# Performance work log

Hardware: AMD Instinct MI355X
Metric: run time of the kernel (lower is better)

Reference implementation:

```python
import jax, jax.numpy as jnp
import numpy as np

BS, CIN, COUT, KS, H, W = 16, 256, 256, 3, 80, 80
HID = CIN // 16   # Attention hidden = in_planes // ratio(16)
K = 5             # len(angle_list)
TEMP = 30.0       # attention temperature

# Spatial permutations replicating AdaptiveAngleConv._rotate_kernel for 3x3 kernels.
# perm[dest_flat] = source_flat (flat = 3*row + col).
_PERMS = {
    45:  np.array([3, 0, 1, 6, 4, 2, 7, 8, 5]),
    90:  np.array([6, 3, 0, 7, 4, 1, 8, 5, 2]),
    135: np.array([7, 6, 3, 8, 4, 0, 5, 2, 1]),
    180: np.array([8, 7, 6, 5, 4, 3, 2, 1, 0]),
}

def _rotate(w, angle):
    o, i = w.shape[:2]
    return w.reshape(o, i, 9)[..., _PERMS[angle]].reshape(o, i, 3, 3)

def setup_inputs() -> dict:
    key = jax.random.key(0)
    ks = jax.random.split(key, 9)
    s = lambda fan: 1.0 / np.sqrt(fan)
    return {
        "x":       jax.random.normal(ks[0], (BS, CIN, H, W), jnp.float32),
        "w_base":  jax.random.normal(ks[1], (COUT, CIN, KS, KS), jnp.float32) * s(CIN * KS * KS),
        "b_base":  jax.random.normal(ks[2], (COUT,), jnp.float32) * 0.1,
        "b_extra": jax.random.normal(ks[3], (K - 1, COUT), jnp.float32) * 0.1,
        "w_net":   jax.random.normal(ks[4], (HID, CIN), jnp.float32) * s(CIN),
        "w_nfc":   jax.random.normal(ks[5], (K, HID), jnp.float32) * s(HID),
        "w_cin":   jax.random.normal(ks[6], (CIN, HID), jnp.float32) * s(HID),
        "w_k2":    jax.random.normal(ks[7], (KS * KS, HID), jnp.float32) * s(HID),
        "w_out":   jax.random.normal(ks[8], (COUT, HID), jnp.float32) * s(HID),
    }

def reference(x, w_base, b_base, b_extra, w_net, w_nfc, w_cin, w_k2, w_out):
    bs = x.shape[0]
    # Attention: global-avg-pool then 1x1 convs == matmuls on pooled vectors
    pooled = x.mean(axis=(2, 3))                                   # [bs, Cin]
    h = jax.nn.relu(pooled @ w_net.T)                              # [bs, HID]
    n_att   = jax.nn.softmax((h @ w_nfc.T) / TEMP, axis=-1)        # [bs, K]
    cin_att = jax.nn.sigmoid(h @ w_cin.T)                          # [bs, Cin]
    k2_att  = jax.nn.sigmoid(h @ w_k2.T).reshape(bs, 1, 1, KS, KS) # [bs,1,1,ks,ks]
    out_att = jax.nn.sigmoid(h @ w_out.T)                          # [bs, Cout]

    # K rotated kernel variants: [K, Cout, Cin, ks, ks]
    k_sum = jnp.stack([w_base, _rotate(w_base, 45), _rotate(w_base, 90),
                       _rotate(w_base, 135), _rotate(w_base, 180)], axis=0)
    b_sum = jnp.concatenate([b_base[None], b_extra], axis=0)       # [K, Cout]

    # Per-sample dynamic weight synthesis
    agg_w = jnp.einsum('bk,koicd->boicd', n_att, k_sum)            # [bs,Cout,Cin,ks,ks]
    agg_w = (agg_w
             * cin_att[:, None, :, None, None]
             * k2_att
             * out_att[:, :, None, None, None])
    agg_b = n_att @ b_sum                                          # [bs, Cout]

    # Per-sample conv (== F.conv2d with groups=bs trick)
    def conv1(xi, wi, bi):
        y = jax.lax.conv_general_dilated(
            xi[None], wi, window_strides=(1, 1), padding=((1, 1), (1, 1)),
            dimension_numbers=('NCHW', 'OIHW', 'NCHW'))[0]
        return y + bi[:, None, None]

    return jax.vmap(conv1)(x, agg_w, agg_b)                        # [bs,Cout,H,W]
```

## Files before the change

### kernel.cpp

```cpp
#include <hip/hip_runtime.h>
#include <hip/hip_bf16.h>
#include <cstdint>
#include <cstddef>

#define BS   16
#define CIN  256
#define COUT 256
#define HID  16
#define KNUM 5
#define TEMP 30.0f
#define NPIX 6400

typedef _Float16 half8 __attribute__((ext_vector_type(8)));
typedef float    f32x4 __attribute__((ext_vector_type(4)));

__device__ __forceinline__ void gload_lds16(const void* g, void* l) {
    __builtin_amdgcn_global_load_lds(
        (const __attribute__((address_space(1))) unsigned int*)g,
        (__attribute__((address_space(3))) unsigned int*)l, 16, 0, 0);
}

__global__ void zero_pool_kernel(float* __restrict__ pooled) {
    pooled[blockIdx.x * 256 + threadIdx.x] = 0.f;
}

__global__ __launch_bounds__(256)
void xpose_kernel(const float* __restrict__ x, _Float16* __restrict__ xt,
                  float* __restrict__ pooled) {
    const int b = blockIdx.y, p0 = blockIdx.x * 64, c = threadIdx.x;
    const float* xp = x + ((size_t)(b * CIN + c)) * NPIX + p0;
    _Float16* tp = xt + ((size_t)b * NPIX + p0) * CIN + c;
    float s = 0.f;
    #pragma unroll
    for (int k0 = 0; k0 < 64; k0 += 16) {
        float4 v[4];
        #pragma unroll
        for (int q = 0; q < 4; ++q) v[q] = *(const float4*)(xp + k0 + q * 4);
        #pragma unroll
        for (int q = 0; q < 4; ++q) {
            s += v[q].x + v[q].y + v[q].z + v[q].w;
            tp[(size_t)(k0 + q * 4 + 0) * CIN] = (_Float16)v[q].x;
            tp[(size_t)(k0 + q * 4 + 1) * CIN] = (_Float16)v[q].y;
            tp[(size_t)(k0 + q * 4 + 2) * CIN] = (_Float16)v[q].z;
            tp[(size_t)(k0 + q * 4 + 3) * CIN] = (_Float16)v[q].w;
        }
    }
    atomicAdd(&pooled[b * CIN + c], s);
}

__global__ void attn_kernel(const float* __restrict__ pooled,
                            const float* __restrict__ b_base,
                            const float* __restrict__ b_extra,
                            const float* __restrict__ w_net,
                            const float* __restrict__ w_nfc,
                            const float* __restrict__ w_cin,
                            const float* __restrict__ w_k2,
                            const float* __restrict__ w_out,
                            float* __restrict__ cin_att,
                            float* __restrict__ out_att,
                            float* __restrict__ agg_b,
                            float* __restrict__ coef,
                            float pool_scale) {
    const int b = blockIdx.x;
    const int t = threadIdx.x;
    __shared__ float sp[CIN];
    __shared__ float sh[HID];
    __shared__ float sn[KNUM];
    __shared__ float sk2[9];

    sp[t] = pooled[b * CIN + t] * pool_scale;
    __syncthreads();

    if (t < HID) {
        float a = 0.f;
        for (int c = 0; c < CIN; ++c) a += sp[c] * w_net[t * CIN + c];
        sh[t] = fmaxf(a, 0.f);
    }
    __syncthreads();

    if (t == 0) {
        float l[KNUM], m = -1e30f;
        for (int k = 0; k < KNUM; ++k) {
            float a = 0.f;
            for (int j = 0; j < HID; ++j) a += sh[j] * w_nfc[k * HID + j];
            l[k] = a / TEMP;
            m = fmaxf(m, l[k]);
        }
        float ssum = 0.f;
        for (int k = 0; k < KNUM; ++k) { l[k] = __expf(l[k] - m); ssum += l[k]; }
        for (int k = 0; k < KNUM; ++k) sn[k] = l[k] / ssum;
    }
    if (t < 9) {
        float a = 0.f;
        for (int j = 0; j < HID; ++j) a += sh[j] * w_k2[t * HID + j];
        sk2[t] = 1.f / (1.f + __expf(-a));
    }
    __syncthreads();

    {
        float a = 0.f, o = 0.f;
        for (int j = 0; j < HID; ++j) {
            a += sh[j] * w_cin[t * HID + j];
            o += sh[j] * w_out[t * HID + j];
        }
        cin_att[b * CIN + t] = 1.f / (1.f + __expf(-a));
        out_att[b * COUT + t] = 1.f / (1.f + __expf(-o));
        float bb = sn[0] * b_base[t];
        for (int k = 1; k < KNUM; ++k) bb += sn[k] * b_extra[(k - 1) * COUT + t];
        agg_b[b * COUT + t] = bb;
    }

    if (t < 81) {
        const int P45[9]  = {3, 0, 1, 6, 4, 2, 7, 8, 5};
        const int P90[9]  = {6, 3, 0, 7, 4, 1, 8, 5, 2};
        const int P135[9] = {7, 6, 3, 8, 4, 0, 5, 2, 1};
        const int P180[9] = {8, 7, 6, 5, 4, 3, 2, 1, 0};
        const int d = t / 9, s = t % 9;
        float c = 0.f;
        if (d == s)        c += sn[0];
        if (P45[d]  == s)  c += sn[1];
        if (P90[d]  == s)  c += sn[2];
        if (P135[d] == s)  c += sn[3];
        if (P180[d] == s)  c += sn[4];
        coef[b * 81 + t] = c * sk2[d];
    }
}

__global__ __launch_bounds__(256)
void wsyn_f16_kernel(const float* __restrict__ w_base,
                     const float* __restrict__ cin_att,
                     const float* __restrict__ out_att,
                     const float* __restrict__ coef,
                     _Float16* __restrict__ wsyn) {
    const int icb = blockIdx.x, og = blockIdx.y, b = blockIdx.z;
    const int t = threadIdx.x;
    const int kb = t >> 6, o_l = t & 63;
    const int o = og * 64 + o_l;
    const int i0 = icb * 32 + kb * 8;

    __shared__ float sc[81];
    if (t < 81) sc[t] = coef[b * 81 + t];
    __syncthreads();

    const float so = out_att[b * COUT + o];
    float wb[8][9], sci[8];
    const float* wp = w_base + ((size_t)o * CIN + i0) * 9;
    #pragma unroll
    for (int j = 0; j < 8; ++j) {
        sci[j] = cin_att[b * CIN + i0 + j] * so;
        #pragma unroll
        for (int s = 0; s < 9; ++s) wb[j][s] = wp[j * 9 + s];
    }
    #pragma unroll
    for (int tap = 0; tap < 9; ++tap) {
        half8 h;
        #pragma unroll
        for (int j = 0; j < 8; ++j) {
            float a = 0.f;
            #pragma unroll
            for (int s = 0; s < 9; ++s) a = fmaf(sc[tap * 9 + s], wb[j][s], a);
            h[j] = (_Float16)(a * sci[j]);
        }
        *(half8*)(wsyn + ((size_t)(b * 8 + icb) * 36 + tap * 4 + kb) * 2048
                        + (size_t)o * 8) = h;
    }
}

__global__ __launch_bounds__(256, 2)
void conv_mfma_kernel(const _Float16* __restrict__ xt,
                      const _Float16* __restrict__ wsyn,
                      const float* __restrict__ agg_b,
                      float* __restrict__ y) {
    const int tile = blockIdx.x;
    const int tc = tile % 5, tr = tile / 5;
    const int og = blockIdx.y;
    const int b = blockIdx.z;

    __shared__ _Float16 wlds[18432];
    __shared__ _Float16 xlds[12960];

    const int t = threadIdx.x;
    const int w = t >> 6, lane = t & 63, l15 = lane & 15, l4 = lane >> 4;
    const int row0 = tr * 16 - 1, col0 = tc * 16 - 1;

    f32x4 acc[4][4];
    const f32x4 z = {0.f, 0.f, 0.f, 0.f};
    #pragma unroll
    for (int a = 0; a < 4; ++a)
        #pragma unroll
        for (int p = 0; p < 4; ++p) acc[a][p] = z;

    for (int icb = 0; icb < 8; ++icb) {
        const _Float16* gw = wsyn + (size_t)(b * 8 + icb) * 73728 + og * 512;
        #pragma unroll
        for (int q = 0; q < 9; ++q) {
            const int L = q * 2048 + t * 8;
            const int tapkb = L >> 9;
            gload_lds16(gw + (size_t)tapkb * 2048 + (L & 511),
                        wlds + q * 2048 + w * 512);
        }
        const _Float16* gx = xt + (size_t)b * NPIX * CIN + icb * 32;
        #pragma unroll
        for (int it = 0; it < 6; ++it) {
            const int idx = t + it * 256;
            if (idx < 1296) {
                const int rc = idx >> 2, part = idx & 3;
                const int rr = rc / 18, cc = rc % 18;
                const int gr = row0 + rr, gc = col0 + cc;
                uint4 v = make_uint4(0u, 0u, 0u, 0u);
                if ((unsigned)gr < 80u && (unsigned)gc < 80u)
                    v = *(const uint4*)(gx + (size_t)(gr * 80 + gc) * CIN + part * 8);
                *(uint4*)((char*)xlds + rc * 80 + part * 16) = v;
            }
        }
        __syncthreads();

        #pragma unroll
        for (int tap = 0; tap < 9; ++tap) {
            const int dh = tap / 3, dw = tap % 3;
            half8 A[4], Bv[4];
            #pragma unroll
            for (int ot = 0; ot < 4; ++ot)
                A[ot] = *(const half8*)(wlds +
                        ((size_t)(tap * 4 + l4) * 64 + ot * 16 + l15) * 8);
            #pragma unroll
            for (int pt = 0; pt < 4; ++pt)
                Bv[pt] = *(const half8*)((const char*)xlds +
                        ((w * 4 + pt + dh) * 18 + l15 + dw) * 80 + l4 * 16);
            #pragma unroll
            for (int ot = 0; ot < 4; ++ot)
                #pragma unroll
                for (int pt = 0; pt < 4; ++pt)
                    acc[ot][pt] = __builtin_amdgcn_mfma_f32_16x16x32_f16(
                        A[ot], Bv[pt], acc[ot][pt], 0, 0, 0);
        }
        __syncthreads();
    }

    const int prow0 = tr * 16 + w * 4;
    #pragma unroll
    for (int ot = 0; ot < 4; ++ot) {
        const int o = og * 64 + ot * 16 + l4 * 4;
        #pragma unroll
        for (int q = 0; q < 4; ++q) {
            const float bv = agg_b[b * COUT + o + q];
            #pragma unroll
            for (int pt = 0; pt < 4; ++pt)
                y[(size_t)(b * COUT + o + q) * NPIX + (prow0 + pt) * 80
                  + tc * 16 + l15] = acc[ot][pt][q] + bv;
        }
    }
}

__global__ void pool_kernel(const float* __restrict__ x, float* __restrict__ pooled) {
    const int bc = blockIdx.x;
    const float* p = x + (size_t)bc * NPIX;
    float s = 0.f;
    for (int i = threadIdx.x; i < NPIX; i += 256) s += p[i];
    #pragma unroll
    for (int off = 32; off; off >>= 1) s += __shfl_down(s, off, 64);
    __shared__ float red[4];
    if ((threadIdx.x & 63) == 0) red[threadIdx.x >> 6] = s;
    __syncthreads();
    if (threadIdx.x == 0)
        pooled[bc] = (red[0] + red[1] + red[2] + red[3]) * (1.f / (float)NPIX);
}

__global__ void wsyn_kernel(const float* __restrict__ w_base,
                            const float* __restrict__ cin_att,
                            const float* __restrict__ out_att,
                            const float* __restrict__ coef,
                            float* __restrict__ wsyn) {
    const int i = blockIdx.x;
    const int o = threadIdx.x;
    __shared__ float sc[BS][81];
    __shared__ float sci[BS];
    for (int l = o; l < BS * 81; l += 256) sc[l / 81][l % 81] = coef[l];
    if (o < BS) sci[o] = cin_att[o * CIN + i];
    __syncthreads();

    float wb[9];
    const float* wp = w_base + ((size_t)o * CIN + i) * 9;
    #pragma unroll
    for (int s = 0; s < 9; ++s) wb[s] = wp[s];

    for (int b = 0; b < BS; ++b) {
        const float scale = sci[b] * out_att[b * COUT + o];
        float* outp = wsyn + (((size_t)b * CIN + i) * 9) * COUT + o;
        #pragma unroll
        for (int d = 0; d < 9; ++d) {
            float a = 0.f;
            #pragma unroll
            for (int s = 0; s < 9; ++s) a += sc[b][d * 9 + s] * wb[s];
            outp[(size_t)d * COUT] = a * scale;
        }
    }
}

__global__ __launch_bounds__(256, 3)
void conv_kernel(const float* __restrict__ x,
                 const float* __restrict__ wsyn,
                 const float* __restrict__ agg_b,
                 float* __restrict__ y) {
    const int tile = blockIdx.x;
    const int tx = tile % 5;
    const int ty = tile / 5;
    const int oBase = blockIdx.y * 64;
    const int b = blockIdx.z;

    __shared__ float xs[4][10][18];
    __shared__ float wsh[4][9][64];

    const int t  = threadIdx.x;
    const int og = t & 15;
    const int oL = og * 4;
    const int pg = t >> 4;
    const int r  = pg >> 1;
    const int c0 = (pg & 1) * 8;

    float acc[4][8];
    #pragma unroll
    for (int a = 0; a < 4; ++a)
        #pragma unroll
        for (int p = 0; p < 8; ++p) acc[a][p] = 0.f;

    const int row0 = ty * 8 - 1;
    const int col0 = tx * 16 - 1;
    const float* xb  = x + (size_t)b * CIN * NPIX;
    const float* wsb = wsyn + (size_t)b * CIN * 9 * COUT + oBase;

    for (int icb = 0; icb < CIN / 4; ++icb) {
        #pragma unroll
        for (int q = 0; q < 3; ++q) {
            const int l = t + q * 256;
            if (l < 720) {
                const int ic  = l / 180;
                const int rem = l % 180;
                const int rr  = rem / 18;
                const int cc  = rem % 18;
                const int gr = row0 + rr, gc = col0 + cc;
                float v = 0.f;
                if ((unsigned)gr < 80u && (unsigned)gc < 80u)
                    v = xb[(size_t)(icb * 4 + ic) * NPIX + gr * 80 + gc];
                ((float*)xs)[l] = v;
            }
        }
        #pragma unroll
        for (int q = 0; q < 9; ++q) {
            const int l = t + q * 256;
            const int ic  = l / 576;
            const int rem = l % 576;
            const int tap = rem / 64;
            const int o   = rem & 63;
            ((float*)wsh)[l] = wsb[(size_t)(icb * 4 + ic) * 9 * COUT + tap * COUT + o];
        }
        __syncthreads();

        #pragma unroll
        for (int ic = 0; ic < 4; ++ic) {
            float xr[3][10];
            #pragma unroll
            for (int dh = 0; dh < 3; ++dh)
                #pragma unroll
                for (int c = 0; c < 10; ++c) xr[dh][c] = xs[ic][r + dh][c0 + c];
            #pragma unroll
            for (int tap = 0; tap < 9; ++tap) {
                const int dh = tap / 3, dw = tap % 3;
                const float4 wv = *(const float4*)&wsh[ic][tap][oL];
                #pragma unroll
                for (int oo = 0; oo < 4; ++oo) {
                    const float wq = (&wv.x)[oo];
                    #pragma unroll
                    for (int p = 0; p < 8; ++p)
                        acc[oo][p] = fmaf(wq, xr[dh][p + dw], acc[oo][p]);
                }
            }
        }
        __syncthreads();
    }

    #pragma unroll
    for (int oo = 0; oo < 4; ++oo) {
        const int o = oBase + oL + oo;
        const float bv = agg_b[b * COUT + o];
        float* yp = y + (size_t)(b * COUT + o) * NPIX + (ty * 8 + r) * 80 + tx * 16 + c0;
        float4 v0 = make_float4(acc[oo][0] + bv, acc[oo][1] + bv,
                                acc[oo][2] + bv, acc[oo][3] + bv);
        float4 v1 = make_float4(acc[oo][4] + bv, acc[oo][5] + bv,
                                acc[oo][6] + bv, acc[oo][7] + bv);
        *(float4*)yp = v0;
        *((float4*)yp + 1) = v1;
    }
}

extern "C" void kernel_launch(void* const* d_in, const int* in_sizes, int n_in,
                              void* d_out, int out_size, void* d_ws, size_t ws_size,
                              hipStream_t stream) {
    const float* x       = (const float*)d_in[0];
    const float* w_base  = (const float*)d_in[1];
    const float* b_base  = (const float*)d_in[2];
    const float* b_extra = (const float*)d_in[3];
    const float* w_net   = (const float*)d_in[4];
    const float* w_nfc   = (const float*)d_in[5];
    const float* w_cin   = (const float*)d_in[6];
    const float* w_k2    = (const float*)d_in[7];
    const float* w_out   = (const float*)d_in[8];
    float* y = (float*)d_out;

    float* ws      = (float*)d_ws;
    float* pooled  = ws;
    float* cin_att = ws + 4096;
    float* out_att = ws + 8192;
    float* agg_b   = ws + 12288;
    float* coef    = ws + 16384;

    const size_t XT_OFF = 131072;
    const size_t WH_OFF = XT_OFF + (size_t)BS * NPIX * CIN * 2;
    const size_t NEED   = WH_OFF + (size_t)BS * 8 * 36 * 2048 * 2;

    if (ws_size >= NEED) {
        _Float16* xt  = (_Float16*)((char*)d_ws + XT_OFF);
        _Float16* wh  = (_Float16*)((char*)d_ws + WH_OFF);
        zero_pool_kernel<<<BS, 256, 0, stream>>>(pooled);
        xpose_kernel<<<dim3(100, BS), 256, 0, stream>>>(x, xt, pooled);
        attn_kernel<<<BS, 256, 0, stream>>>(pooled, b_base, b_extra, w_net, w_nfc,
                                            w_cin, w_k2, w_out,
                                            cin_att, out_att, agg_b, coef,
                                            1.f / (float)NPIX);
        wsyn_f16_kernel<<<dim3(8, 4, BS), 256, 0, stream>>>(w_base, cin_att,
                                                            out_att, coef, wh);
        conv_mfma_kernel<<<dim3(25, 4, BS), 256, 0, stream>>>(xt, wh, agg_b, y);
    } else {
        float* wsyn = ws + 17680;
        pool_kernel<<<BS * CIN, 256, 0, stream>>>(x, pooled);
        attn_kernel<<<BS, 256, 0, stream>>>(pooled, b_base, b_extra, w_net, w_nfc,
                                            w_cin, w_k2, w_out,
                                            cin_att, out_att, agg_b, coef, 1.f);
        wsyn_kernel<<<CIN, 256, 0, stream>>>(w_base, cin_att, out_att, coef, wsyn);
        conv_kernel<<<dim3(50, 4, BS), 256, 0, stream>>>(x, wsyn, agg_b, y);
    }
}
```

Baseline: 358.7 us.

## Stream weights from global into registers and prefetch next input block in conv

The conv kernel no longer stages synthesized weights in LDS. It loads each tap's A fragments straight from global memory into registers, one tap ahead, and prefetches the next input-channel block of the transposed activations into registers while the MFMAs run. Dropping the weight LDS buffer lets the launch bound rise to three blocks per CU. Separately, the transpose kernel is rewritten so each thread writes contiguous half8 channel vectors, and pooling moves back to a separate reduction kernel with no atomics. The cost is an extra full read of x for pooling, uncoalesced strided reads in the transpose, more register pressure, and a second barrier per iteration.

Result: slower. 592.3 us (+65.1%).

```diff
diff --git a/kernel.cpp b/kernel.cpp
--- a/kernel.cpp
+++ b/kernel.cpp
@@ -14,38 +14,38 @@
 typedef _Float16 half8 __attribute__((ext_vector_type(8)));
 typedef float    f32x4 __attribute__((ext_vector_type(4)));
 
-__device__ __forceinline__ void gload_lds16(const void* g, void* l) {
-    __builtin_amdgcn_global_load_lds(
-        (const __attribute__((address_space(1))) unsigned int*)g,
-        (__attribute__((address_space(3))) unsigned int*)l, 16, 0, 0);
-}
-
-__global__ void zero_pool_kernel(float* __restrict__ pooled) {
-    pooled[blockIdx.x * 256 + threadIdx.x] = 0.f;
+__global__ void pool_kernel(const float* __restrict__ x, float* __restrict__ pooled) {
+    const int bc = blockIdx.x;
+    const float* p = x + (size_t)bc * NPIX;
+    float s = 0.f;
+    for (int i = threadIdx.x; i < NPIX; i += 256) s += p[i];
+    #pragma unroll
+    for (int off = 32; off; off >>= 1) s += __shfl_down(s, off, 64);
+    __shared__ float red[4];
+    if ((threadIdx.x & 63) == 0) red[threadIdx.x >> 6] = s;
+    __syncthreads();
+    if (threadIdx.x == 0)
+        pooled[bc] = (red[0] + red[1] + red[2] + red[3]) * (1.f / (float)NPIX);
 }
 
 __global__ __launch_bounds__(256)
-void xpose_kernel(const float* __restrict__ x, _Float16* __restrict__ xt,
-                  float* __restrict__ pooled) {
-    const int b = blockIdx.y, p0 = blockIdx.x * 64, c = threadIdx.x;
-    const float* xp = x + ((size_t)(b * CIN + c)) * NPIX + p0;
-    _Float16* tp = xt + ((size_t)b * NPIX + p0) * CIN + c;
-    float s = 0.f;
-    #pragma unroll
-    for (int k0 = 0; k0 < 64; k0 += 16) {
-        float4 v[4];
-        #pragma unroll
-        for (int q = 0; q < 4; ++q) v[q] = *(const float4*)(xp + k0 + q * 4);
-        #pragma unroll
-        for (int q = 0; q < 4; ++q) {
-            s += v[q].x + v[q].y + v[q].z + v[q].w;
-            tp[(size_t)(k0 + q * 4 + 0) * CIN] = (_Float16)v[q].x;
-            tp[(size_t)(k0 + q * 4 + 1) * CIN] = (_Float16)v[q].y;
-            tp[(size_t)(k0 + q * 4 + 2) * CIN] = (_Float16)v[q].z;
-            tp[(size_t)(k0 + q * 4 + 3) * CIN] = (_Float16)v[q].w;
-        }
-    }
-    atomicAdd(&pooled[b * CIN + c], s);
+void xpose_kernel(const float* __restrict__ x, _Float16* __restrict__ xt) {
+    const int b = blockIdx.y, p0 = blockIdx.x * 64;
+    const int pl = threadIdx.x & 63, cq = threadIdx.x >> 6;
+    const int px = p0 + pl;
+    const float* xb = x + (size_t)b * CIN * NPIX + px;
+    _Float16* tp = xt + ((size_t)b * NPIX + px) * CIN;
+    #pragma unroll
+    for (int k = 0; k < 8; ++k) {
+        const int c0 = cq * 64 + k * 8;
+        float v[8];
+        #pragma unroll
+        for (int j = 0; j < 8; ++j) v[j] = xb[(size_t)(c0 + j) * NPIX];
+        half8 h;
+        #pragma unroll
+        for (int j = 0; j < 8; ++j) h[j] = (_Float16)v[j];
+        *(half8*)(tp + c0) = h;
+    }
 }
 
 __global__ void attn_kernel(const float* __restrict__ pooled,
@@ -59,8 +59,7 @@
                             float* __restrict__ cin_att,
                             float* __restrict__ out_att,
                             float* __restrict__ agg_b,
-                            float* __restrict__ coef,
-                            float pool_scale) {
+                            float* __restrict__ coef) {
     const int b = blockIdx.x;
     const int t = threadIdx.x;
     __shared__ float sp[CIN];
@@ -68,7 +67,7 @@
     __shared__ float sn[KNUM];
     __shared__ float sk2[9];
 
-    sp[t] = pooled[b * CIN + t] * pool_scale;
+    sp[t] = pooled[b * CIN + t];
     __syncthreads();
 
     if (t < HID) {
@@ -166,7 +165,7 @@
     }
 }
 
-__global__ __launch_bounds__(256, 2)
+__global__ __launch_bounds__(256, 3)
 void conv_mfma_kernel(const _Float16* __restrict__ xt,
                       const _Float16* __restrict__ wsyn,
                       const float* __restrict__ agg_b,
@@ -176,12 +175,26 @@
     const int og = blockIdx.y;
     const int b = blockIdx.z;
 
-    __shared__ _Float16 wlds[18432];
     __shared__ _Float16 xlds[12960];
 
     const int t = threadIdx.x;
-    const int w = t >> 6, lane = t & 63, l15 = lane & 15, l4 = lane >> 4;
+    const int lane = t & 63, l15 = lane & 15, l4 = lane >> 4, w = t >> 6;
     const int row0 = tr * 16 - 1, col0 = tc * 16 - 1;
+
+    int px_base[6], lds_byte[6];
+    #pragma unroll
+    for (int it = 0; it < 6; ++it) {
+        const int idx = t + it * 256;
+        px_base[it] = -1; lds_byte[it] = 0;
+        if (idx < 1296) {
+            const int rc = idx >> 2, part = idx & 3;
+            const int rr = rc / 18, cc = rc % 18;
+            const int gr = row0 + rr, gc = col0 + cc;
+            lds_byte[it] = rc * 80 + part * 16;
+            if ((unsigned)gr < 80u && (unsigned)gc < 80u)
+                px_base[it] = (gr * 80 + gc) * CIN + part * 8;
+        }
+    }
 
     f32x4 acc[4][4];
     const f32x4 z = {0.f, 0.f, 0.f, 0.f};
@@ -190,39 +203,54 @@
         #pragma unroll
         for (int p = 0; p < 4; ++p) acc[a][p] = z;
 
+    const _Float16* gx  = xt + (size_t)b * NPIX * CIN;
+    const _Float16* gw0 = wsyn + (size_t)b * 8 * 73728 + og * 512
+                        + (size_t)l4 * 2048 + (size_t)l15 * 8;
+
+    {
+        uint4 xr[6];
+        #pragma unroll
+        for (int it = 0; it < 6; ++it) {
+            xr[it] = make_uint4(0u, 0u, 0u, 0u);
+            if (px_base[it] >= 0)
+                xr[it] = *(const uint4*)(gx + px_base[it]);
+        }
+        #pragma unroll
+        for (int it = 0; it < 6; ++it)
+            if (t + it * 256 < 1296)
+                *(uint4*)((char*)xlds + lds_byte[it]) = xr[it];
+    }
+    __syncthreads();
+
     for (int icb = 0; icb < 8; ++icb) {
-        const _Float16* gw = wsyn + (size_t)(b * 8 + icb) * 73728 + og * 512;
-        #pragma unroll
-        for (int q = 0; q < 9; ++q) {
-            const int L = q * 2048 + t * 8;
-            const int tapkb = L >> 9;
-            gload_lds16(gw + (size_t)tapkb * 2048 + (L & 511),
-                        wlds + q * 2048 + w * 512);
-        }
-        const _Float16* gx = xt + (size_t)b * NPIX * CIN + icb * 32;
-        #pragma unroll
-        for (int it = 0; it < 6; ++it) {
-            const int idx = t + it * 256;
-            if (idx < 1296) {
-                const int rc = idx >> 2, part = idx & 3;
-                const int rr = rc / 18, cc = rc % 18;
-                const int gr = row0 + rr, gc = col0 + cc;
-                uint4 v = make_uint4(0u, 0u, 0u, 0u);
-                if ((unsigned)gr < 80u && (unsigned)gc < 80u)
-                    v = *(const uint4*)(gx + (size_t)(gr * 80 + gc) * CIN + part * 8);
-                *(uint4*)((char*)xlds + rc * 80 + part * 16) = v;
-            }
-        }
-        __syncthreads();
-
+        uint4 xn[6];
+        #pragma unroll
+        for (int it = 0; it < 6; ++it) xn[it] = make_uint4(0u, 0u, 0u, 0u);
+        if (icb < 7) {
+            #pragma unroll
+            for (int it = 0; it < 6; ++it)
+                if (px_base[it] >= 0)
+                    xn[it] = *(const uint4*)(gx + px_base[it] + (icb + 1) * 32);
+        }
+
+        const _Float16* gw = gw0 + (size_t)icb * 73728;
+        half8 An[4];
+        #pragma unroll
+        for (int ot = 0; ot < 4; ++ot)
+            An[ot] = *(const half8*)(gw + (size_t)ot * 128);
         #pragma unroll
         for (int tap = 0; tap < 9; ++tap) {
             const int dh = tap / 3, dw = tap % 3;
-            half8 A[4], Bv[4];
-            #pragma unroll
-            for (int ot = 0; ot < 4; ++ot)
-                A[ot] = *(const half8*)(wlds +
-                        ((size_t)(tap * 4 + l4) * 64 + ot * 16 + l15) * 8);
+            half8 A[4];
+            #pragma unroll
+            for (int ot = 0; ot < 4; ++ot) A[ot] = An[ot];
+            if (tap < 8) {
+                #pragma unroll
+                for (int ot = 0; ot < 4; ++ot)
+                    An[ot] = *(const half8*)(gw + (size_t)(tap + 1) * 8192
+                                                + (size_t)ot * 128);
+            }
+            half8 Bv[4];
             #pragma unroll
             for (int pt = 0; pt < 4; ++pt)
                 Bv[pt] = *(const half8*)((const char*)xlds +
@@ -235,6 +263,13 @@
                         A[ot], Bv[pt], acc[ot][pt], 0, 0, 0);
         }
         __syncthreads();
+        if (icb < 7) {
+            #pragma unroll
+            for (int it = 0; it < 6; ++it)
+                if (t + it * 256 < 1296)
+                    *(uint4*)((char*)xlds + lds_byte[it]) = xn[it];
+        }
+        __syncthreads();
     }
 
     const int prow0 = tr * 16 + w * 4;
@@ -250,20 +285,6 @@
                   + tc * 16 + l15] = acc[ot][pt][q] + bv;
         }
     }
-}
-
-__global__ void pool_kernel(const float* __restrict__ x, float* __restrict__ pooled) {
-    const int bc = blockIdx.x;
-    const float* p = x + (size_t)bc * NPIX;
-    float s = 0.f;
-    for (int i = threadIdx.x; i < NPIX; i += 256) s += p[i];
-    #pragma unroll
-    for (int off = 32; off; off >>= 1) s += __shfl_down(s, off, 64);
-    __shared__ float red[4];
-    if ((threadIdx.x & 63) == 0) red[threadIdx.x >> 6] = s;
-    __syncthreads();
-    if (threadIdx.x == 0)
-        pooled[bc] = (red[0] + red[1] + red[2] + red[3]) * (1.f / (float)NPIX);
 }
 
 __global__ void wsyn_kernel(const float* __restrict__ w_base,
@@ -421,12 +442,11 @@
     if (ws_size >= NEED) {
         _Float16* xt  = (_Float16*)((char*)d_ws + XT_OFF);
         _Float16* wh  = (_Float16*)((char*)d_ws + WH_OFF);
-        zero_pool_kernel<<<BS, 256, 0, stream>>>(pooled);
-        xpose_kernel<<<dim3(100, BS), 256, 0, stream>>>(x, xt, pooled);
+        pool_kernel<<<BS * CIN, 256, 0, stream>>>(x, pooled);
+        xpose_kernel<<<dim3(100, BS), 256, 0, stream>>>(x, xt);
         attn_kernel<<<BS, 256, 0, stream>>>(pooled, b_base, b_extra, w_net, w_nfc,
                                             w_cin, w_k2, w_out,
-                                            cin_att, out_att, agg_b, coef,
-                                            1.f / (float)NPIX);
+                                            cin_att, out_att, agg_b, coef);
         wsyn_f16_kernel<<<dim3(8, 4, BS), 256, 0, stream>>>(w_base, cin_att,
                                                             out_att, coef, wh);
         conv_mfma_kernel<<<dim3(25, 4, BS), 256, 0, stream>>>(xt, wh, agg_b, y);
@@ -435,7 +455,7 @@
         pool_kernel<<<BS * CIN, 256, 0, stream>>>(x, pooled);
         attn_kernel<<<BS, 256, 0, stream>>>(pooled, b_base, b_extra, w_net, w_nfc,
                                             w_cin, w_k2, w_out,
-                                            cin_att, out_att, agg_b, coef, 1.f);
+                                            cin_att, out_att, agg_b, coef);
         wsyn_kernel<<<CIN, 256, 0, stream>>>(w_base, cin_att, out_att, coef, wsyn);
         conv_kernel<<<dim3(50, 4, BS), 256, 0, stream>>>(x, wsyn, agg_b, y);
     }
```

## Transpose input via LDS tile, separate pooling kernel, reorder conv x-tile LDS layout

Applied to the files above, without the earlier changes.

The transpose kernel now stages a 256-channel by 64-pixel tile in shared memory so that global stores become 16-byte contiguous half8 writes instead of scattered 2-byte stores. Pooling moves out to a separate reduction kernel, which removes the atomics and the zeroing launch but reads x a second time. The conv kernel's x tile in LDS is rearranged into a channel-part-major layout with no padding, to cut bank conflicts on the B-operand reads and shrink LDS use.

Measured after the change: 374.3 us. 4.3% more time.

```diff
diff --git a/kernel.cpp b/kernel.cpp
--- a/kernel.cpp
+++ b/kernel.cpp
@@ -12,6 +12,7 @@
 #define NPIX 6400
 
 typedef _Float16 half8 __attribute__((ext_vector_type(8)));
+typedef _Float16 half4 __attribute__((ext_vector_type(4)));
 typedef float    f32x4 __attribute__((ext_vector_type(4)));
 
 __device__ __forceinline__ void gload_lds16(const void* g, void* l) {
@@ -20,32 +21,50 @@
         (__attribute__((address_space(3))) unsigned int*)l, 16, 0, 0);
 }
 
-__global__ void zero_pool_kernel(float* __restrict__ pooled) {
-    pooled[blockIdx.x * 256 + threadIdx.x] = 0.f;
+__global__ void pool_kernel(const float* __restrict__ x, float* __restrict__ pooled) {
+    const int bc = blockIdx.x;
+    const float* p = x + (size_t)bc * NPIX;
+    float s = 0.f;
+    for (int i = threadIdx.x; i < NPIX; i += 256) s += p[i];
+    #pragma unroll
+    for (int off = 32; off; off >>= 1) s += __shfl_down(s, off, 64);
+    __shared__ float red[4];
+    if ((threadIdx.x & 63) == 0) red[threadIdx.x >> 6] = s;
+    __syncthreads();
+    if (threadIdx.x == 0)
+        pooled[bc] = (red[0] + red[1] + red[2] + red[3]) * (1.f / (float)NPIX);
 }
 
 __global__ __launch_bounds__(256)
-void xpose_kernel(const float* __restrict__ x, _Float16* __restrict__ xt,
-                  float* __restrict__ pooled) {
-    const int b = blockIdx.y, p0 = blockIdx.x * 64, c = threadIdx.x;
-    const float* xp = x + ((size_t)(b * CIN + c)) * NPIX + p0;
-    _Float16* tp = xt + ((size_t)b * NPIX + p0) * CIN + c;
-    float s = 0.f;
-    #pragma unroll
-    for (int k0 = 0; k0 < 64; k0 += 16) {
-        float4 v[4];
-        #pragma unroll
-        for (int q = 0; q < 4; ++q) v[q] = *(const float4*)(xp + k0 + q * 4);
-        #pragma unroll
-        for (int q = 0; q < 4; ++q) {
-            s += v[q].x + v[q].y + v[q].z + v[q].w;
-            tp[(size_t)(k0 + q * 4 + 0) * CIN] = (_Float16)v[q].x;
-            tp[(size_t)(k0 + q * 4 + 1) * CIN] = (_Float16)v[q].y;
-            tp[(size_t)(k0 + q * 4 + 2) * CIN] = (_Float16)v[q].z;
-            tp[(size_t)(k0 + q * 4 + 3) * CIN] = (_Float16)v[q].w;
-        }
-    }
-    atomicAdd(&pooled[b * CIN + c], s);
+void xpose_kernel(const float* __restrict__ x, _Float16* __restrict__ xt) {
+    const int b = blockIdx.y, p0 = blockIdx.x * 64;
+    __shared__ _Float16 tile[256 * 68];
+
+    const int t = threadIdx.x;
+    const int l16 = t & 15, cq = t >> 4;
+
+    #pragma unroll
+    for (int it = 0; it < 16; ++it) {
+        const int c = it * 16 + cq;
+        const float4 v = *(const float4*)(x + ((size_t)(b * CIN + c)) * NPIX
+                                            + p0 + l16 * 4);
+        half4 h;
+        h[0] = (_Float16)v.x; h[1] = (_Float16)v.y;
+        h[2] = (_Float16)v.z; h[3] = (_Float16)v.w;
+        *(half4*)(tile + c * 68 + l16 * 4) = h;
+    }
+    __syncthreads();
+
+    const int lpx = t >> 2, ch = t & 3;
+    _Float16* tp = xt + ((size_t)b * NPIX + p0 + lpx) * CIN;
+    #pragma unroll
+    for (int j = 0; j < 8; ++j) {
+        const int c0 = ch * 8 + j * 32;
+        half8 h;
+        #pragma unroll
+        for (int i = 0; i < 8; ++i) h[i] = tile[(c0 + i) * 68 + lpx];
+        *(half8*)(tp + c0) = h;
+    }
 }
 
 __global__ void attn_kernel(const float* __restrict__ pooled,
@@ -59,8 +78,7 @@
                             float* __restrict__ cin_att,
                             float* __restrict__ out_att,
                             float* __restrict__ agg_b,
-                            float* __restrict__ coef,
-                            float pool_scale) {
+                            float* __restrict__ coef) {
     const int b = blockIdx.x;
     const int t = threadIdx.x;
     __shared__ float sp[CIN];
@@ -68,7 +86,7 @@
     __shared__ float sn[KNUM];
     __shared__ float sk2[9];
 
-    sp[t] = pooled[b * CIN + t] * pool_scale;
+    sp[t] = pooled[b * CIN + t];
     __syncthreads();
 
     if (t < HID) {
@@ -177,7 +195,7 @@
     const int b = blockIdx.z;
 
     __shared__ _Float16 wlds[18432];
-    __shared__ _Float16 xlds[12960];
+    __shared__ _Float16 xlds[10368];
 
     const int t = threadIdx.x;
     const int w = t >> 6, lane = t & 63, l15 = lane & 15, l4 = lane >> 4;
@@ -210,7 +228,7 @@
                 uint4 v = make_uint4(0u, 0u, 0u, 0u);
                 if ((unsigned)gr < 80u && (unsigned)gc < 80u)
                     v = *(const uint4*)(gx + (size_t)(gr * 80 + gc) * CIN + part * 8);
-                *(uint4*)((char*)xlds + rc * 80 + part * 16) = v;
+                *(uint4*)((char*)xlds + rr * 1152 + part * 288 + cc * 16) = v;
             }
         }
         __syncthreads();
@@ -226,7 +244,7 @@
             #pragma unroll
             for (int pt = 0; pt < 4; ++pt)
                 Bv[pt] = *(const half8*)((const char*)xlds +
-                        ((w * 4 + pt + dh) * 18 + l15 + dw) * 80 + l4 * 16);
+                        (((w * 4 + pt + dh) * 4 + l4) * 18 + l15 + dw) * 16);
             #pragma unroll
             for (int ot = 0; ot < 4; ++ot)
                 #pragma unroll
@@ -250,20 +268,6 @@
                   + tc * 16 + l15] = acc[ot][pt][q] + bv;
         }
     }
-}
-
-__global__ void pool_kernel(const float* __restrict__ x, float* __restrict__ pooled) {
-    const int bc = blockIdx.x;
-    const float* p = x + (size_t)bc * NPIX;
-    float s = 0.f;
-    for (int i = threadIdx.x; i < NPIX; i += 256) s += p[i];
-    #pragma unroll
-    for (int off = 32; off; off >>= 1) s += __shfl_down(s, off, 64);
-    __shared__ float red[4];
-    if ((threadIdx.x & 63) == 0) red[threadIdx.x >> 6] = s;
-    __syncthreads();
-    if (threadIdx.x == 0)
-        pooled[bc] = (red[0] + red[1] + red[2] + red[3]) * (1.f / (float)NPIX);
 }
 
 __global__ void wsyn_kernel(const float* __restrict__ w_base,
@@ -421,12 +425,11 @@
     if (ws_size >= NEED) {
         _Float16* xt  = (_Float16*)((char*)d_ws + XT_OFF);
         _Float16* wh  = (_Float16*)((char*)d_ws + WH_OFF);
-        zero_pool_kernel<<<BS, 256, 0, stream>>>(pooled);
-        xpose_kernel<<<dim3(100, BS), 256, 0, stream>>>(x, xt, pooled);
+        pool_kernel<<<BS * CIN, 256, 0, stream>>>(x, pooled);
+        xpose_kernel<<<dim3(100, BS), 256, 0, stream>>>(x, xt);
         attn_kernel<<<BS, 256, 0, stream>>>(pooled, b_base, b_extra, w_net, w_nfc,
                                             w_cin, w_k2, w_out,
-                                            cin_att, out_att, agg_b, coef,
-                                            1.f / (float)NPIX);
+                                            cin_att, out_att, agg_b, coef);
         wsyn_f16_kernel<<<dim3(8, 4, BS), 256, 0, stream>>>(w_base, cin_att,
                                                             out_att, coef, wh);
         conv_mfma_kernel<<<dim3(25, 4, BS), 256, 0, stream>>>(xt, wh, agg_b, y);
@@ -435,7 +438,7 @@
         pool_kernel<<<BS * CIN, 256, 0, stream>>>(x, pooled);
         attn_kernel<<<BS, 256, 0, stream>>>(pooled, b_base, b_extra, w_net, w_nfc,
                                             w_cin, w_k2, w_out,
-                                            cin_att, out_att, agg_b, coef, 1.f);
+                                            cin_att, out_att, agg_b, coef);
         wsyn_kernel<<<CIN, 256, 0, stream>>>(w_base, cin_att, out_att, coef, wsyn);
         conv_kernel<<<dim3(50, 4, BS), 256, 0, stream>>>(x, wsyn, agg_b, y);
     }
```

## Block transposed activations by 32-channel groups and restage via LDS tile

Applied to the files above, without the earlier changes.

The transpose kernel now stages a 32-channel by 256-pixel tile in LDS, writes each pixel's 32 channels as contiguous 16-byte vectors, and reduces the pool sum with wave shuffles before one atomic per channel. The transposed activation layout becomes [b][icb][pix][32] instead of [b][pix][256], so the conv kernel reads contiguous 64-byte rows per pixel. The conv LDS x tile is repacked without the 80-byte padding into a part-major layout, which shrinks shared memory and changes the bank pattern of the MFMA operand loads. The aim is to replace the old scattered 2-byte global stores and cut conv load and LDS overhead, but the new LDS layout may introduce bank conflicts.

Measured after the change: 354.9 us. Within noise of the previous version (-1.1%).

```diff
diff --git a/kernel.cpp b/kernel.cpp
--- a/kernel.cpp
+++ b/kernel.cpp
@@ -12,6 +12,7 @@
 #define NPIX 6400
 
 typedef _Float16 half8 __attribute__((ext_vector_type(8)));
+typedef _Float16 half4 __attribute__((ext_vector_type(4)));
 typedef float    f32x4 __attribute__((ext_vector_type(4)));
 
 __device__ __forceinline__ void gload_lds16(const void* g, void* l) {
@@ -27,25 +28,42 @@
 __global__ __launch_bounds__(256)
 void xpose_kernel(const float* __restrict__ x, _Float16* __restrict__ xt,
                   float* __restrict__ pooled) {
-    const int b = blockIdx.y, p0 = blockIdx.x * 64, c = threadIdx.x;
-    const float* xp = x + ((size_t)(b * CIN + c)) * NPIX + p0;
-    _Float16* tp = xt + ((size_t)b * NPIX + p0) * CIN + c;
+    const int p0 = blockIdx.x * 256, icb = blockIdx.y, b = blockIdx.z;
+    __shared__ _Float16 tile[32 * 258];
+
+    const int t = threadIdx.x;
+    const int ch = t >> 3, fq = t & 7;
+    const float* xp = x + ((size_t)(b * CIN + icb * 32 + ch)) * NPIX + p0;
+
     float s = 0.f;
     #pragma unroll
-    for (int k0 = 0; k0 < 64; k0 += 16) {
-        float4 v[4];
-        #pragma unroll
-        for (int q = 0; q < 4; ++q) v[q] = *(const float4*)(xp + k0 + q * 4);
-        #pragma unroll
-        for (int q = 0; q < 4; ++q) {
-            s += v[q].x + v[q].y + v[q].z + v[q].w;
-            tp[(size_t)(k0 + q * 4 + 0) * CIN] = (_Float16)v[q].x;
-            tp[(size_t)(k0 + q * 4 + 1) * CIN] = (_Float16)v[q].y;
-            tp[(size_t)(k0 + q * 4 + 2) * CIN] = (_Float16)v[q].z;
-            tp[(size_t)(k0 + q * 4 + 3) * CIN] = (_Float16)v[q].w;
-        }
-    }
-    atomicAdd(&pooled[b * CIN + c], s);
+    for (int it = 0; it < 8; ++it) {
+        const int px0 = (fq + it * 8) * 4;
+        const float4 v = *(const float4*)(xp + px0);
+        s += v.x + v.y + v.z + v.w;
+        half4 h;
+        h[0] = (_Float16)v.x; h[1] = (_Float16)v.y;
+        h[2] = (_Float16)v.z; h[3] = (_Float16)v.w;
+        *(half4*)(tile + ch * 258 + px0) = h;
+    }
+    s += __shfl_xor(s, 1, 64);
+    s += __shfl_xor(s, 2, 64);
+    s += __shfl_xor(s, 4, 64);
+    if (fq == 0) atomicAdd(&pooled[b * CIN + icb * 32 + ch], s);
+    __syncthreads();
+
+    const int px = t;
+    _Float16 vals[32];
+    #pragma unroll
+    for (int c = 0; c < 32; ++c) vals[c] = tile[c * 258 + px];
+    _Float16* tp = xt + ((size_t)(b * 8 + icb) * NPIX + p0 + px) * 32;
+    #pragma unroll
+    for (int q = 0; q < 4; ++q) {
+        half8 h;
+        #pragma unroll
+        for (int j = 0; j < 8; ++j) h[j] = vals[q * 8 + j];
+        *(half8*)(tp + q * 8) = h;
+    }
 }
 
 __global__ void attn_kernel(const float* __restrict__ pooled,
@@ -177,7 +195,7 @@
     const int b = blockIdx.z;
 
     __shared__ _Float16 wlds[18432];
-    __shared__ _Float16 xlds[12960];
+    __shared__ _Float16 xlds[10368];
 
     const int t = threadIdx.x;
     const int w = t >> 6, lane = t & 63, l15 = lane & 15, l4 = lane >> 4;
@@ -199,7 +217,7 @@
             gload_lds16(gw + (size_t)tapkb * 2048 + (L & 511),
                         wlds + q * 2048 + w * 512);
         }
-        const _Float16* gx = xt + (size_t)b * NPIX * CIN + icb * 32;
+        const _Float16* gx = xt + (size_t)(b * 8 + icb) * NPIX * 32;
         #pragma unroll
         for (int it = 0; it < 6; ++it) {
             const int idx = t + it * 256;
@@ -209,8 +227,8 @@
                 const int gr = row0 + rr, gc = col0 + cc;
                 uint4 v = make_uint4(0u, 0u, 0u, 0u);
                 if ((unsigned)gr < 80u && (unsigned)gc < 80u)
-                    v = *(const uint4*)(gx + (size_t)(gr * 80 + gc) * CIN + part * 8);
-                *(uint4*)((char*)xlds + rc * 80 + part * 16) = v;
+                    v = *(const uint4*)(gx + (size_t)(gr * 80 + gc) * 32 + part * 8);
+                *(uint4*)((char*)xlds + rr * 1152 + part * 288 + cc * 16) = v;
             }
         }
         __syncthreads();
@@ -226,7 +244,7 @@
             #pragma unroll
             for (int pt = 0; pt < 4; ++pt)
                 Bv[pt] = *(const half8*)((const char*)xlds +
-                        ((w * 4 + pt + dh) * 18 + l15 + dw) * 80 + l4 * 16);
+                        (((w * 4 + pt + dh) * 4 + l4) * 18 + l15 + dw) * 16);
             #pragma unroll
             for (int ot = 0; ot < 4; ++ot)
                 #pragma unroll
@@ -422,7 +440,7 @@
         _Float16* xt  = (_Float16*)((char*)d_ws + XT_OFF);
         _Float16* wh  = (_Float16*)((char*)d_ws + WH_OFF);
         zero_pool_kernel<<<BS, 256, 0, stream>>>(pooled);
-        xpose_kernel<<<dim3(100, BS), 256, 0, stream>>>(x, xt, pooled);
+        xpose_kernel<<<dim3(25, 8, BS), 256, 0, stream>>>(x, xt, pooled);
         attn_kernel<<<BS, 256, 0, stream>>>(pooled, b_base, b_extra, w_net, w_nfc,
                                             w_cin, w_k2, w_out,
                                             cin_att, out_att, agg_b, coef,
```
